# Performance work log

Measured on AMD Instinct MI355X. Metric: run time of the kernel, lower is better.

## Reference

```python
import jax, jax.numpy as jnp
import numpy as np

B, S, D = 2, 2048, 2048
H, HKV, DH = 32, 8, 64
WIN = 1024  # sliding_window
SCALE = 1.0 / np.sqrt(DH)
NEG_INF = -1e30


def setup_inputs() -> dict:
    key = jax.random.key(0)
    ks = jax.random.split(key, 6)
    w = 0.02
    inp = {
        "hidden_states": jax.random.normal(ks[0], (B, S, D), jnp.float32),
        "Wq": jax.random.normal(ks[1], (D, D), jnp.float32) * w,
        "bq": jnp.zeros((D,), jnp.float32),
        "Wk": jax.random.normal(ks[2], (HKV * DH, D), jnp.float32) * w,
        "bk": jnp.zeros((HKV * DH,), jnp.float32),
        "Wv": jax.random.normal(ks[3], (HKV * DH, D), jnp.float32) * w,
        "bv": jnp.zeros((HKV * DH,), jnp.float32),
        "Wo": jax.random.normal(ks[4], (D, D), jnp.float32) * w,
        "bo": jnp.zeros((D,), jnp.float32),
        # reset_parameters (default init): 1 / logspace(0, 7, H, base=2)
        "alibi_slopes": 1.0 / jnp.exp2(jnp.linspace(0.0, 7.0, H)).astype(jnp.float32),
    }
    return inp


def reference(hidden_states, Wq, bq, Wk, bk, Wv, bv, Wo, bo, alibi_slopes):
    x = hidden_states
    q = (x @ Wq.T + bq).reshape(B, S, H, DH).transpose(0, 2, 1, 3)      # [B,H,S,DH]
    k = (x @ Wk.T + bk).reshape(B, S, HKV, DH).transpose(0, 2, 1, 3)    # [B,HKV,S,DH]
    v = (x @ Wv.T + bv).reshape(B, S, HKV, DH).transpose(0, 2, 1, 3)
    # GQA: each kv head serves H//HKV consecutive query heads
    group = H // HKV
    k = jnp.repeat(k, group, axis=1)  # [B,H,S,DH]
    v = jnp.repeat(v, group, axis=1)

    scores = jnp.einsum("bhqd,bhkd->bhqk", q, k) * SCALE  # [B,H,S,S]
    i = jnp.arange(S)[:, None]
    j = jnp.arange(S)[None, :]
    rel = (j - i).astype(jnp.float32)  # <= 0 for attended past positions
    # ALiBi: slope * (j - i) -> linear penalty on distance
    bias = alibi_slopes[:, None, None] * rel  # [H,S,S]
    mask = (j <= i) & ((i - j) < WIN)  # [S,S]
    scores = jnp.where(mask[None, None], scores + bias[None], NEG_INF)
    probs = jax.nn.softmax(scores, axis=-1)
    out = jnp.einsum("bhqk,bhkd->bhqd", probs, v)  # [B,H,S,DH]
    out = out.transpose(0, 2, 1, 3).reshape(B, S, D)
    return out @ Wo.T + bo
```

## Files before the change

### kernel.cpp

```cpp
#include <hip/hip_runtime.h>
#include <hip/hip_bf16.h>
#include <stdint.h>
#include <type_traits>

typedef unsigned short ushort_t;
typedef __bf16 bf16x8 __attribute__((ext_vector_type(8)));
typedef __bf16 bf16x4 __attribute__((ext_vector_type(4)));
typedef short s16x4 __attribute__((ext_vector_type(4)));
typedef unsigned short u16x8 __attribute__((ext_vector_type(8)));
typedef float f32x4 __attribute__((ext_vector_type(4)));

#define MFMA_BF16(a, b, c) __builtin_amdgcn_mfma_f32_16x16x32_bf16((a), (b), (c), 0, 0, 0)

#define GLD_LDS(gptr, lptr) \
    __builtin_amdgcn_global_load_lds((const __attribute__((address_space(1))) void*)(gptr), \
                                     (__attribute__((address_space(3))) void*)(lptr), 16, 0, 0)

static __device__ __forceinline__ float bf2f(__hip_bfloat16 x) { return __bfloat162float(x); }
static __device__ __forceinline__ ushort_t f2bfbits(float f) {
    __hip_bfloat16 h = __float2bfloat16(f);
    return *(ushort_t*)&h;
}
static __device__ __forceinline__ float fmax3(float a, float b, float c) {
    return fmaxf(fmaxf(a, b), c);
}

static __device__ __forceinline__ f32x4 MFMA16(bf16x4 a, bf16x4 b, f32x4 c) {
#if __has_builtin(__builtin_amdgcn_mfma_f32_16x16x16_bf16)
    return __builtin_amdgcn_mfma_f32_16x16x16_bf16(a, b, c, 0, 0, 0);
#elif __has_builtin(__builtin_amdgcn_mfma_f32_16x16x16bf16_1k)
    union { bf16x4 b4; s16x4 s4; } ua, ub;
    ua.b4 = a; ub.b4 = b;
    return __builtin_amdgcn_mfma_f32_16x16x16bf16_1k(ua.s4, ub.s4, c, 0, 0, 0);
#else
    const bf16x4 z = {(__bf16)0.f, (__bf16)0.f, (__bf16)0.f, (__bf16)0.f};
    bf16x8 a8 = __builtin_shufflevector(a, z, 0, 1, 2, 3, 4, 5, 6, 7);
    bf16x8 b8 = __builtin_shufflevector(b, z, 0, 1, 2, 3, 4, 5, 6, 7);
    return MFMA_BF16(a8, b8, c);
#endif
}

static __device__ __forceinline__ bf16x4 pack4(float a, float b, float c, float d) {
    union { ushort4 u; bf16x4 v; } r;
    r.u = make_ushort4(f2bfbits(a), f2bfbits(b), f2bfbits(c), f2bfbits(d));
    return r.v;
}

template <typename T>
static __device__ __forceinline__ void storeT(T* p, float v);
template <>
__device__ __forceinline__ void storeT<float>(float* p, float v) { *p = v; }
template <>
__device__ __forceinline__ void storeT<__hip_bfloat16>(__hip_bfloat16* p, float v) {
    *p = __float2bfloat16(v);
}

__global__ void detect_kernel(const ushort_t* __restrict__ X,
                              const void* bq, const void* bk, const void* bv,
                              const void* bo, const void* slopes,
                              int* flag, float* slopesF, float* bqF,
                              float* bkF, float* bvF, float* boF) {
    __shared__ int cnt_s;
    if (threadIdx.x == 0) cnt_s = 0;
    __syncthreads();
    int cnt = 0;
    for (int i = threadIdx.x; i < 8192; i += 256) {
        ushort_t u = X[2 * i];
        int ex = (u >> 7) & 0xFF;
        if (ex >= 0xC0) cnt++;
    }
    for (int off = 1; off < 64; off <<= 1) cnt += __shfl_xor(cnt, off);
    if ((threadIdx.x & 63) == 0) atomicAdd(&cnt_s, cnt);
    __syncthreads();
    const bool f32 = cnt_s > 100;
    if (threadIdx.x == 0) *flag = f32 ? 1 : 0;
    auto conv = [&](const void* src, float* dst, int n) {
        for (int i = threadIdx.x; i < n; i += 256)
            dst[i] = f32 ? ((const float*)src)[i]
                         : __bfloat162float(((const __hip_bfloat16*)src)[i]);
    };
    conv(bq, bqF, 2048);
    conv(bk, bkF, 512);
    conv(bv, bvF, 512);
    conv(bo, boF, 2048);
    conv(slopes, slopesF, 32);
}

__global__ __launch_bounds__(256) void cvt_kernel(const int* __restrict__ flag,
                                                  const void* __restrict__ src,
                                                  ushort_t* __restrict__ dst, int n4) {
    const bool f32 = (*flag == 1);
    const int stride = gridDim.x * 256;
    for (int i = blockIdx.x * 256 + threadIdx.x; i < n4; i += stride) {
        if (f32) {
            float4 f = ((const float4*)src)[i];
            ((ushort4*)dst)[i] =
                make_ushort4(f2bfbits(f.x), f2bfbits(f.y), f2bfbits(f.z), f2bfbits(f.w));
        } else {
            ((ushort4*)dst)[i] = ((const ushort4*)src)[i];
        }
    }
}

__device__ __forceinline__ void stage_tile(const __hip_bfloat16* __restrict__ M, int K,
                                           int k0, ushort_t* lds, int tid) {
    const int wave = tid >> 6, lane = tid & 63;
    const int srow = lane >> 3;
    const int scol = ((lane & 7) ^ srow) * 8;
#pragma unroll
    for (int t = 0; t < 4; ++t) {
        const int chunk = wave * 4 + t;
        GLD_LDS((const ushort_t*)M + (size_t)(chunk * 8 + srow) * K + k0 + scol,
                lds + chunk * 512);
    }
}

__device__ __forceinline__ void stage_tile(const float* __restrict__ M, int K,
                                           int k0, ushort_t* lds, int tid) {
#pragma unroll
    for (int q = 0; q < 8; ++q) {
        const int idx = q * 256 + tid;
        const int row = idx >> 4;
        const int c4 = (idx & 15) * 4;
        float4 f = *(const float4*)(M + (size_t)row * K + k0 + c4);
        const int dcol = (((c4 >> 3) ^ (row & 7)) * 8) + (c4 & 7);
        *(ushort4*)(lds + row * 64 + dcol) =
            make_ushort4(f2bfbits(f.x), f2bfbits(f.y), f2bfbits(f.z), f2bfbits(f.w));
    }
}

template <typename TA, typename TW, typename TC>
__device__ __forceinline__ void gemm_tile(const TA* __restrict__ A,
                                          const TW* __restrict__ W,
                                          const float* __restrict__ biasF,
                                          TC* __restrict__ C, int K, int ldc) {
    __shared__ __align__(16) ushort_t As[128 * 64];
    __shared__ __align__(16) ushort_t Bs[128 * 64];
    const int tid = threadIdx.x;
    const int wave = tid >> 6, lane = tid & 63;
    const int quad = lane >> 4, l15 = lane & 15;
    const int wm = (wave >> 1) * 64, wn = (wave & 1) * 64;
    const int sw = l15 & 7;

    f32x4 acc[4][4];
#pragma unroll
    for (int i = 0; i < 4; ++i)
#pragma unroll
        for (int j = 0; j < 4; ++j) acc[i][j] = {0.f, 0.f, 0.f, 0.f};

    for (int k0 = 0; k0 < K; k0 += 64) {
        stage_tile(A, K, k0, As, tid);
        stage_tile(W, K, k0, Bs, tid);
        __syncthreads();
#pragma unroll
        for (int kk = 0; kk < 2; ++kk) {
            const int chs = ((kk * 4 + quad) ^ sw) * 8;
            bf16x8 af[4], bfr[4];
#pragma unroll
            for (int mi = 0; mi < 4; ++mi)
                af[mi] = *(const bf16x8*)(As + (wm + mi * 16 + l15) * 64 + chs);
#pragma unroll
            for (int ni = 0; ni < 4; ++ni)
                bfr[ni] = *(const bf16x8*)(Bs + (wn + ni * 16 + l15) * 64 + chs);
#pragma unroll
            for (int mi = 0; mi < 4; ++mi)
#pragma unroll
                for (int ni = 0; ni < 4; ++ni)
                    acc[mi][ni] = MFMA_BF16(af[mi], bfr[ni], acc[mi][ni]);
        }
        __syncthreads();
    }
#pragma unroll
    for (int mi = 0; mi < 4; ++mi) {
#pragma unroll
        for (int ni = 0; ni < 4; ++ni) {
            const int col = wn + ni * 16 + l15;
            const float bv = biasF[col];
#pragma unroll
            for (int r = 0; r < 4; ++r) {
                const int row = wm + mi * 16 + quad * 4 + r;
                storeT(C + (size_t)row * ldc + col, acc[mi][ni][r] + bv);
            }
        }
    }
}

__global__ __launch_bounds__(256, 2) void qkv_fast(
    const __hip_bfloat16* __restrict__ X,
    const __hip_bfloat16* __restrict__ Wq, const __hip_bfloat16* __restrict__ Wk,
    const __hip_bfloat16* __restrict__ Wv, const float* __restrict__ bqF,
    const float* __restrict__ bkF, const float* __restrict__ bvF,
    __hip_bfloat16* __restrict__ Qb, __hip_bfloat16* __restrict__ Kb,
    __hip_bfloat16* __restrict__ Vb) {
    const int nt = blockIdx.x, mt = blockIdx.y;
    const __hip_bfloat16* W;
    const float* bias;
    __hip_bfloat16* C;
    int ldc, colbase;
    if (nt < 16)      { W = Wq; bias = bqF; C = Qb; ldc = 2048; colbase = nt * 128; }
    else if (nt < 20) { W = Wk; bias = bkF; C = Kb; ldc = 512;  colbase = (nt - 16) * 128; }
    else              { W = Wv; bias = bvF; C = Vb; ldc = 512;  colbase = (nt - 20) * 128; }
    gemm_tile(X + (size_t)mt * 128 * 2048, W + (size_t)colbase * 2048, bias + colbase,
              C + (size_t)mt * 128 * ldc + colbase, 2048, ldc);
}

__global__ __launch_bounds__(256, 2) void oproj_fast(
    const __hip_bfloat16* __restrict__ A, const __hip_bfloat16* __restrict__ Wo,
    const float* __restrict__ boF, float* __restrict__ C) {
    gemm_tile(A + (size_t)blockIdx.y * 128 * 2048,
              Wo + (size_t)blockIdx.x * 128 * 2048, boF + blockIdx.x * 128,
              C + (size_t)blockIdx.y * 128 * 2048 + blockIdx.x * 128, 2048, 2048);
}

__global__ __launch_bounds__(256) void vtrans_kernel(const ushort_t* __restrict__ Vb,
                                                     ushort_t* __restrict__ Vt) {
    const int blk = blockIdx.x;
    const int bh = blk >> 6;
    const int sc = blk & 63;
    const int tid = threadIdx.x;
    const int dh = tid & 63;
    const int s0 = sc * 32 + (tid >> 6) * 8;
    const int b = bh >> 3, hkv = bh & 7;
    u16x8 vv;
#pragma unroll
    for (int e = 0; e < 8; ++e)
        vv[e] = Vb[((size_t)(b * 2048 + s0 + e)) * 512 + hkv * 64 + dh];
    *(u16x8*)(Vt + ((size_t)(bh * 64 + dh)) * 2048 + s0) = vv;
}

template <bool F32>
__global__ __launch_bounds__(256, 2) void qkv_kernel(
    const int* __restrict__ flag, const void* __restrict__ Xv,
    const void* __restrict__ Wqv, const void* __restrict__ Wkv,
    const void* __restrict__ Wvv, const float* __restrict__ bqF,
    const float* __restrict__ bkF, const float* __restrict__ bvF,
    __hip_bfloat16* __restrict__ Qb, __hip_bfloat16* __restrict__ Kb,
    __hip_bfloat16* __restrict__ Vb) {
    if ((*flag == 1) != F32) return;
    using T = typename std::conditional<F32, float, __hip_bfloat16>::type;
    const T* X = (const T*)Xv;
    const int nt = blockIdx.x, mt = blockIdx.y;
    const T* W;
    const float* bias;
    __hip_bfloat16* C;
    int ldc, colbase;
    if (nt < 16)      { W = (const T*)Wqv; bias = bqF; C = Qb; ldc = 2048; colbase = nt * 128; }
    else if (nt < 20) { W = (const T*)Wkv; bias = bkF; C = Kb; ldc = 512;  colbase = (nt - 16) * 128; }
    else              { W = (const T*)Wvv; bias = bvF; C = Vb; ldc = 512;  colbase = (nt - 20) * 128; }
    gemm_tile(X + (size_t)mt * 128 * 2048, W + (size_t)colbase * 2048, bias + colbase,
              C + (size_t)mt * 128 * ldc + colbase, 2048, ldc);
}

template <bool F32>
__global__ __launch_bounds__(256, 2) void oproj_kernel(
    const int* __restrict__ flag, const __hip_bfloat16* __restrict__ A,
    const void* __restrict__ Wov, const float* __restrict__ boF,
    float* __restrict__ C) {
    if ((*flag == 1) != F32) return;
    using T = typename std::conditional<F32, float, __hip_bfloat16>::type;
    gemm_tile(A + (size_t)blockIdx.y * 128 * 2048,
              (const T*)Wov + (size_t)blockIdx.x * 128 * 2048, boF + blockIdx.x * 128,
              C + (size_t)blockIdx.y * 128 * 2048 + blockIdx.x * 128, 2048, 2048);
}

__global__ __launch_bounds__(256, 4) void attn4_kernel(
    const __hip_bfloat16* __restrict__ Qg, const __hip_bfloat16* __restrict__ Kg,
    const ushort_t* __restrict__ Vt, const float* __restrict__ slopesF,
    __hip_bfloat16* __restrict__ Og) {
    constexpr int S = 2048, WIN = 1024;
    constexpr float LOG2E = 1.44269504f;
    constexpr float SCALE2 = 0.125f * LOG2E;
    constexpr float NEGBIG = -3e38f;
    __shared__ __align__(16) ushort_t K0s[64 * 64];
    __shared__ __align__(16) ushort_t V0s[64 * 64];
    __shared__ __align__(16) ushort_t K1s[64 * 64];
    __shared__ __align__(16) ushort_t V1s[64 * 64];

    const int p = blockIdx.x;
    const int xcd = p & 7;
    const int slot = p >> 3;
    const int bh = (slot >> 7) * 8 + xcd;
    const int h2 = (slot >> 5) & 3;
    const int qt = 31 - (slot & 31);
    const int b = bh >> 3, hkv = bh & 7;
    const int h = hkv * 4 + h2;
    const int i0 = qt * 64;

    const int tid = threadIdx.x;
    const int wave = tid >> 6, lane = tid & 63;
    const int quad = lane >> 4, l15 = lane & 15;
    const int jl = lane >> 3, cc = lane & 7;
    const float slope2 = slopesF[h] * LOG2E;

    const ushort_t* kbase = (const ushort_t*)Kg + (size_t)(b * S) * 512 + hkv * 64;
    const ushort_t* vbase = Vt + ((size_t)bh * 64) * 2048;

    auto stage = [&](int j0, ushort_t* Ks, ushort_t* Vs) {
        const int row0 = wave * 16;
#pragma unroll
        for (int t = 0; t < 2; ++t) {
            const int r = row0 + t * 8 + jl;
            GLD_LDS(kbase + (size_t)(j0 + r) * 512 + ((cc ^ (r & 7)) * 8),
                    Ks + (row0 + t * 8) * 64);
            GLD_LDS(vbase + (size_t)r * 2048 + j0 + ((cc ^ (r & 7)) * 8),
                    Vs + (row0 + t * 8) * 64);
        }
    };

    const int i = i0 + wave * 16 + l15;
    const __hip_bfloat16* qbase = Qg + ((size_t)(b * S + i)) * 2048 + h * 64;
    bf16x8 aq0 = *(const bf16x8*)(qbase + quad * 8);
    bf16x8 aq1 = *(const bf16x8*)(qbase + 32 + quad * 8);

    union { ushort4 u; bf16x4 v; } onesu;
    onesu.u = make_ushort4(0x3F80, 0x3F80, 0x3F80, 0x3F80);
    const bf16x4 onesf = onesu.v;

    f32x4 oaccT[4];
#pragma unroll
    for (int ni = 0; ni < 4; ++ni) oaccT[ni] = {0.f, 0.f, 0.f, 0.f};
    f32x4 lacc = {0.f, 0.f, 0.f, 0.f};
    float m_i = -1e30f;

    auto compute = [&](int j0, const ushort_t* Ks, const ushort_t* Vs, bool masked) {
        f32x4 st[4];
#pragma unroll
        for (int ni = 0; ni < 4; ++ni) st[ni] = {0.f, 0.f, 0.f, 0.f};
#pragma unroll
        for (int kk = 0; kk < 2; ++kk) {
            const bf16x8 aqk = kk ? aq1 : aq0;
#pragma unroll
            for (int ni = 0; ni < 4; ++ni) {
                const int row = ni * 16 + l15;
                bf16x8 kf = *(const bf16x8*)(Ks + row * 64 + ((kk * 4 + quad) ^ (row & 7)) * 8);
                st[ni] = MFMA_BF16(kf, aqk, st[ni]);
            }
        }
        float sv[4][4];
#pragma unroll
        for (int ni = 0; ni < 4; ++ni)
#pragma unroll
            for (int r = 0; r < 4; ++r) {
                const int rel = (j0 + ni * 16 + quad * 4 + r) - i;
                sv[ni][r] = fmaf(st[ni][r], SCALE2, slope2 * (float)rel);
            }
        if (masked) {
#pragma unroll
            for (int ni = 0; ni < 4; ++ni)
#pragma unroll
                for (int r = 0; r < 4; ++r) {
                    const int rel = (j0 + ni * 16 + quad * 4 + r) - i;
                    if (!((unsigned)(-rel) < (unsigned)WIN)) sv[ni][r] = NEGBIG;
                }
        }
        float mx = fmax3(fmax3(sv[0][0], sv[0][1], sv[0][2]),
                         fmax3(sv[0][3], sv[1][0], sv[1][1]),
                         fmax3(sv[1][2], sv[1][3], sv[2][0]));
        float my = fmax3(fmax3(sv[2][1], sv[2][2], sv[2][3]),
                         fmax3(sv[3][0], sv[3][1], sv[3][2]), sv[3][3]);
        mx = fmaxf(mx, my);
        mx = fmaxf(mx, __shfl_xor(mx, 16));
        mx = fmaxf(mx, __shfl_xor(mx, 32));
        if (!__all(mx <= m_i + 8.f)) {
            const float mn = fmaxf(m_i, mx);
            const float alpha = exp2f(m_i - mn);
            m_i = mn;
#pragma unroll
            for (int ni = 0; ni < 4; ++ni)
#pragma unroll
                for (int r = 0; r < 4; ++r) oaccT[ni][r] *= alpha;
            lacc[0] *= alpha;
        }
        float pv[4][4];
#pragma unroll
        for (int ni = 0; ni < 4; ++ni)
#pragma unroll
            for (int r = 0; r < 4; ++r) pv[ni][r] = exp2f(sv[ni][r] - m_i);
        bf16x4 pf[4];
#pragma unroll
        for (int c = 0; c < 4; ++c) pf[c] = pack4(pv[c][0], pv[c][1], pv[c][2], pv[c][3]);
#pragma unroll
        for (int c = 0; c < 4; ++c) lacc = MFMA16(onesf, pf[c], lacc);
#pragma unroll
        for (int ni = 0; ni < 4; ++ni) {
            const int row = ni * 16 + l15;
#pragma unroll
            for (int c = 0; c < 4; ++c) {
                const int cj = c * 2 + (quad >> 1);
                bf16x4 vf = *(const bf16x4*)(Vs + row * 64 + ((cj ^ (row & 7)) * 8) +
                                             (quad & 1) * 4);
                oaccT[ni] = MFMA16(vf, pf[c], oaccT[ni]);
            }
        }
    };

    const int jt_lo = (i0 - WIN + 1) > 0 ? ((i0 - WIN + 1) >> 6) : 0;
    int jt = jt_lo;
    stage(jt * 64, K0s, V0s);
    for (;;) {
        __syncthreads();
        if (jt < qt) stage((jt + 1) * 64, K1s, V1s);
        compute(jt * 64, K0s, V0s, (jt == qt) || (qt - jt >= 16));
        if (++jt > qt) break;
        __syncthreads();
        if (jt < qt) stage((jt + 1) * 64, K0s, V0s);
        compute(jt * 64, K1s, V1s, (jt == qt) || (qt - jt >= 16));
        if (++jt > qt) break;
    }
    const float inv = 1.0f / lacc[0];
    __hip_bfloat16* obase = Og + ((size_t)(b * S + i)) * 2048 + h * 64;
#pragma unroll
    for (int ni = 0; ni < 4; ++ni) {
        ushort4 o4 = make_ushort4(f2bfbits(oaccT[ni][0] * inv), f2bfbits(oaccT[ni][1] * inv),
                                  f2bfbits(oaccT[ni][2] * inv), f2bfbits(oaccT[ni][3] * inv));
        *(ushort4*)((ushort_t*)obase + ni * 16 + quad * 4) = o4;
    }
}

__global__ __launch_bounds__(256, 2) void attn_kernel(
    const __hip_bfloat16* __restrict__ Qg, const __hip_bfloat16* __restrict__ Kg,
    const __hip_bfloat16* __restrict__ Vg, const float* __restrict__ slopesF,
    __hip_bfloat16* __restrict__ Og) {
    constexpr int S = 2048, WIN = 1024;
    constexpr float SCALE = 0.125f;
    constexpr float LOG2E = 1.44269504f;
    __shared__ __align__(16) ushort_t P_lds[64 * 72];
    __shared__ __align__(16) ushort_t Vts[64 * 72];

    const int tile = blockIdx.x;
    const int qt = tile & 31;
    const int h = (tile >> 5) & 31;
    const int b = tile >> 10;
    const int i0 = qt * 64;
    const int hkv = h >> 2;
    const int tid = threadIdx.x;
    const int wave = tid >> 6, lane = tid & 63;
    const int quad = lane >> 4, l15 = lane & 15;
    const float slope = slopesF[h];

    const int qrow = i0 + wave * 16 + l15;
    const __hip_bfloat16* qbase = Qg + ((size_t)(b * S + qrow)) * 2048 + h * 64;
    bf16x8 aq[2];
    aq[0] = *(const bf16x8*)(qbase + quad * 8);
    aq[1] = *(const bf16x8*)(qbase + 32 + quad * 8);

    f32x4 oacc[4];
#pragma unroll
    for (int ni = 0; ni < 4; ++ni) oacc[ni] = {0.f, 0.f, 0.f, 0.f};
    float m_i[4], l_i[4];
#pragma unroll
    for (int r = 0; r < 4; ++r) { m_i[r] = -1e30f; l_i[r] = 0.f; }

    const int jt_lo = (i0 - WIN + 1) > 0 ? ((i0 - WIN + 1) >> 6) : 0;
    for (int jt = jt_lo; jt <= qt; ++jt) {
        const int j0 = jt * 64;
#pragma unroll
        for (int it = 0; it < 2; ++it) {
            const int j = it * 32 + (tid >> 3);
            const int dh0 = (tid & 7) * 8;
            u16x8 vv = *(const u16x8*)(Vg + ((size_t)(b * S + j0 + j)) * 512 + hkv * 64 + dh0);
#pragma unroll
            for (int e = 0; e < 8; ++e) Vts[(dh0 + e) * 72 + j] = vv[e];
        }
        f32x4 sacc[4];
#pragma unroll
        for (int ni = 0; ni < 4; ++ni) sacc[ni] = {0.f, 0.f, 0.f, 0.f};
#pragma unroll
        for (int kk = 0; kk < 2; ++kk) {
#pragma unroll
            for (int ni = 0; ni < 4; ++ni) {
                bf16x8 bkf = *(const bf16x8*)(Kg + ((size_t)(b * S + j0 + ni * 16 + l15)) * 512 +
                                              hkv * 64 + kk * 32 + quad * 8);
                sacc[ni] = MFMA_BF16(aq[kk], bkf, sacc[ni]);
            }
        }
#pragma unroll
        for (int r = 0; r < 4; ++r) {
            const int i = i0 + wave * 16 + quad * 4 + r;
            float sv[4];
            float rowmax = -1e30f;
#pragma unroll
            for (int ni = 0; ni < 4; ++ni) {
                const int j = j0 + ni * 16 + l15;
                float s = sacc[ni][r] * SCALE + slope * (float)(j - i);
                const bool valid = (j <= i) && ((i - j) < WIN);
                s = valid ? s : -1e30f;
                sv[ni] = s;
                rowmax = fmaxf(rowmax, s);
            }
#pragma unroll
            for (int off = 1; off < 16; off <<= 1)
                rowmax = fmaxf(rowmax, __shfl_xor(rowmax, off));
            const float mn = fmaxf(m_i[r], rowmax);
            const float alpha = exp2f((m_i[r] - mn) * LOG2E);
            float rowsum = 0.f;
#pragma unroll
            for (int ni = 0; ni < 4; ++ni) {
                const float p = (sv[ni] > -1e29f) ? exp2f((sv[ni] - mn) * LOG2E) : 0.f;
                P_lds[(wave * 16 + quad * 4 + r) * 72 + ni * 16 + l15] = f2bfbits(p);
                rowsum += p;
            }
#pragma unroll
            for (int off = 1; off < 16; off <<= 1) rowsum += __shfl_xor(rowsum, off);
            l_i[r] = l_i[r] * alpha + rowsum;
            m_i[r] = mn;
#pragma unroll
            for (int ni = 0; ni < 4; ++ni) oacc[ni][r] *= alpha;
        }
        __syncthreads();
#pragma unroll
        for (int kk = 0; kk < 2; ++kk) {
            bf16x8 ap = *(const bf16x8*)(P_lds + (wave * 16 + l15) * 72 + kk * 32 + quad * 8);
#pragma unroll
            for (int ni = 0; ni < 4; ++ni) {
                bf16x8 bvf = *(const bf16x8*)(Vts + (ni * 16 + l15) * 72 + kk * 32 + quad * 8);
                oacc[ni] = MFMA_BF16(ap, bvf, oacc[ni]);
            }
        }
        __syncthreads();
    }
#pragma unroll
    for (int ni = 0; ni < 4; ++ni) {
#pragma unroll
        for (int r = 0; r < 4; ++r) {
            const int srow = i0 + wave * 16 + quad * 4 + r;
            const float v = oacc[ni][r] / l_i[r];
            Og[((size_t)(b * S + srow)) * 2048 + h * 64 + ni * 16 + l15] = __float2bfloat16(v);
        }
    }
}

extern "C" void kernel_launch(void* const* d_in, const int* in_sizes, int n_in,
                              void* d_out, int out_size, void* d_ws, size_t ws_size,
                              hipStream_t stream) {
    (void)in_sizes; (void)n_in; (void)out_size;
    const void* X  = d_in[0];
    const void* Wq = d_in[1];
    const void* bq = d_in[2];
    const void* Wk = d_in[3];
    const void* bk = d_in[4];
    const void* Wv = d_in[5];
    const void* bv = d_in[6];
    const void* Wo = d_in[7];
    const void* bo = d_in[8];
    const void* sl = d_in[9];
    float* outp = (float*)d_out;

    char* ws = (char*)d_ws;
    const size_t SZ_X  = (size_t)4096 * 2048 * 2;
    const size_t SZ_WQ = (size_t)2048 * 2048 * 2;
    const size_t SZ_WK = (size_t)512 * 2048 * 2;
    const size_t SZ_Q  = SZ_X;
    const size_t SZ_K  = (size_t)4096 * 512 * 2;
    const size_t FAST_NEED = SZ_X + SZ_WQ + 2 * SZ_WK + SZ_Q + 2 * SZ_K + 65536;

    if (ws_size >= FAST_NEED) {
        size_t o = 0;
        __hip_bfloat16* Xb  = (__hip_bfloat16*)(ws + o); o += SZ_X;
        __hip_bfloat16* Wqb = (__hip_bfloat16*)(ws + o); o += SZ_WQ;
        __hip_bfloat16* Wkb = (__hip_bfloat16*)(ws + o); o += SZ_WK;
        __hip_bfloat16* Wvb = (__hip_bfloat16*)(ws + o); o += SZ_WK;
        __hip_bfloat16* Qb  = (__hip_bfloat16*)(ws + o); o += SZ_Q;
        __hip_bfloat16* Kb  = (__hip_bfloat16*)(ws + o); o += SZ_K;
        __hip_bfloat16* Vb  = (__hip_bfloat16*)(ws + o); o += SZ_K;
        __hip_bfloat16* Ab  = Xb;
        __hip_bfloat16* Wob = Wqb;
        ushort_t*       Vtg = (ushort_t*)Wkb;
        int*   flag    = (int*)(ws + o);
        float* slopesF = (float*)(ws + o + 1024);
        float* bqF     = (float*)(ws + o + 4096);
        float* bkF     = bqF + 2048;
        float* bvF     = bkF + 512;
        float* boF     = bvF + 512;

        detect_kernel<<<1, 256, 0, stream>>>((const ushort_t*)X, bq, bk, bv, bo, sl,
                                             flag, slopesF, bqF, bkF, bvF, boF);
        cvt_kernel<<<2048, 256, 0, stream>>>(flag, X,  (ushort_t*)Xb,  4096 * 2048 / 4);
        cvt_kernel<<<2048, 256, 0, stream>>>(flag, Wq, (ushort_t*)Wqb, 2048 * 2048 / 4);
        cvt_kernel<<<512,  256, 0, stream>>>(flag, Wk, (ushort_t*)Wkb, 512 * 2048 / 4);
        cvt_kernel<<<512,  256, 0, stream>>>(flag, Wv, (ushort_t*)Wvb, 512 * 2048 / 4);
        qkv_fast<<<dim3(24, 32), 256, 0, stream>>>(Xb, Wqb, Wkb, Wvb, bqF, bkF, bvF,
                                                   Qb, Kb, Vb);
        vtrans_kernel<<<1024, 256, 0, stream>>>((const ushort_t*)Vb, Vtg);
        cvt_kernel<<<2048, 256, 0, stream>>>(flag, Wo, (ushort_t*)Wob, 2048 * 2048 / 4);
        attn4_kernel<<<dim3(2048), 256, 0, stream>>>(Qb, Kb, Vtg, slopesF, Ab);
        oproj_fast<<<dim3(16, 32), 256, 0, stream>>>(Ab, Wob, boF, outp);
    } else {
        const size_t MB = 1024 * 1024;
        __hip_bfloat16* Qb = (__hip_bfloat16*)(ws);
        __hip_bfloat16* Kb = (__hip_bfloat16*)(ws + 16 * MB);
        __hip_bfloat16* Vb = (__hip_bfloat16*)(ws + 20 * MB);
        __hip_bfloat16* Ab = (__hip_bfloat16*)(ws + 24 * MB);
        int*   flag    = (int*)(ws + 40 * MB);
        float* slopesF = (float*)(ws + 40 * MB + 1024);
        float* bqF     = (float*)(ws + 40 * MB + 4096);
        float* bkF     = bqF + 2048;
        float* bvF     = bkF + 512;
        float* boF     = bvF + 512;

        detect_kernel<<<1, 256, 0, stream>>>((const ushort_t*)X, bq, bk, bv, bo, sl,
                                             flag, slopesF, bqF, bkF, bvF, boF);
        qkv_kernel<false><<<dim3(24, 32), 256, 0, stream>>>(flag, X, Wq, Wk, Wv,
                                                            bqF, bkF, bvF, Qb, Kb, Vb);
        qkv_kernel<true><<<dim3(24, 32), 256, 0, stream>>>(flag, X, Wq, Wk, Wv,
                                                           bqF, bkF, bvF, Qb, Kb, Vb);
        attn_kernel<<<dim3(2048), 256, 0, stream>>>(Qb, Kb, Vb, slopesF, Ab);
        oproj_kernel<false><<<dim3(16, 32), 256, 0, stream>>>(flag, Ab, Wo, boF, outp);
        oproj_kernel<true><<<dim3(16, 32), 256, 0, stream>>>(flag, Ab, Wo, boF, outp);
    }
}
```

Measured before the change: 340.2 us.

## Widen attention blocks to 128 query rows, fuse input conversions, raise GEMM occupancy

The attention kernel now runs 512-thread blocks covering 128 query rows (two 64-row tiles), so each staged K/V tile in LDS is shared by eight waves instead of four, which halves K/V global traffic per query. Each wave skips key tiles that fall outside its own causal and sliding-window range. The four separate fp32-to-bf16 conversion launches for X, Wq, Wk and Wv are merged into one kernel to cut launch overhead. The GEMM launch bounds are raised to 3 blocks per CU, which may force register spilling. The wider attention block also adds idle waves at the edges of the window.

```diff
diff --git a/kernel.cpp b/kernel.cpp
--- a/kernel.cpp
+++ b/kernel.cpp
@@ -102,6 +102,39 @@
     }
 }
 
+__global__ __launch_bounds__(256) void cvt4_kernel(const int* __restrict__ flag,
+                                                   const void* __restrict__ X,
+                                                   const void* __restrict__ Wq,
+                                                   const void* __restrict__ Wk,
+                                                   const void* __restrict__ Wv,
+                                                   ushort_t* __restrict__ Xb,
+                                                   ushort_t* __restrict__ Wqb,
+                                                   ushort_t* __restrict__ Wkb,
+                                                   ushort_t* __restrict__ Wvb) {
+    const bool f32 = (*flag == 1);
+    constexpr int nX = 4096 * 2048 / 4;
+    constexpr int nWq = 2048 * 2048 / 4;
+    constexpr int nWk = 512 * 2048 / 4;
+    constexpr int total = nX + nWq + 2 * nWk;
+    const int stride = gridDim.x * 256;
+    for (int i = blockIdx.x * 256 + threadIdx.x; i < total; i += stride) {
+        const void* src;
+        ushort_t* dst;
+        int off;
+        if (i < nX)                 { src = X;  dst = Xb;  off = i; }
+        else if (i < nX + nWq)      { src = Wq; dst = Wqb; off = i - nX; }
+        else if (i < nX + nWq + nWk){ src = Wk; dst = Wkb; off = i - nX - nWq; }
+        else                        { src = Wv; dst = Wvb; off = i - nX - nWq - nWk; }
+        if (f32) {
+            float4 f = ((const float4*)src)[off];
+            ((ushort4*)dst)[off] =
+                make_ushort4(f2bfbits(f.x), f2bfbits(f.y), f2bfbits(f.z), f2bfbits(f.w));
+        } else {
+            ((ushort4*)dst)[off] = ((const ushort4*)src)[off];
+        }
+    }
+}
+
 __device__ __forceinline__ void stage_tile(const __hip_bfloat16* __restrict__ M, int K,
                                            int k0, ushort_t* lds, int tid) {
     const int wave = tid >> 6, lane = tid & 63;
@@ -185,7 +218,7 @@
     }
 }
 
-__global__ __launch_bounds__(256, 2) void qkv_fast(
+__global__ __launch_bounds__(256, 3) void qkv_fast(
     const __hip_bfloat16* __restrict__ X,
     const __hip_bfloat16* __restrict__ Wq, const __hip_bfloat16* __restrict__ Wk,
     const __hip_bfloat16* __restrict__ Wv, const float* __restrict__ bqF,
@@ -204,7 +237,7 @@
               C + (size_t)mt * 128 * ldc + colbase, 2048, ldc);
 }
 
-__global__ __launch_bounds__(256, 2) void oproj_fast(
+__global__ __launch_bounds__(256, 3) void oproj_fast(
     const __hip_bfloat16* __restrict__ A, const __hip_bfloat16* __restrict__ Wo,
     const float* __restrict__ boF, float* __restrict__ C) {
     gemm_tile(A + (size_t)blockIdx.y * 128 * 2048,
@@ -263,7 +296,7 @@
               C + (size_t)blockIdx.y * 128 * 2048 + blockIdx.x * 128, 2048, 2048);
 }
 
-__global__ __launch_bounds__(256, 4) void attn4_kernel(
+__global__ __launch_bounds__(512, 8) void attn4_kernel(
     const __hip_bfloat16* __restrict__ Qg, const __hip_bfloat16* __restrict__ Kg,
     const ushort_t* __restrict__ Vt, const float* __restrict__ slopesF,
     __hip_bfloat16* __restrict__ Og) {
@@ -279,32 +312,28 @@
     const int p = blockIdx.x;
     const int xcd = p & 7;
     const int slot = p >> 3;
-    const int bh = (slot >> 7) * 8 + xcd;
-    const int h2 = (slot >> 5) & 3;
-    const int qt = 31 - (slot & 31);
+    const int bh = (slot >> 6) * 8 + xcd;
+    const int h2 = (slot >> 4) & 3;
+    const int qt2 = 15 - (slot & 15);
     const int b = bh >> 3, hkv = bh & 7;
     const int h = hkv * 4 + h2;
-    const int i0 = qt * 64;
+    const int i0 = qt2 * 128;
 
     const int tid = threadIdx.x;
     const int wave = tid >> 6, lane = tid & 63;
     const int quad = lane >> 4, l15 = lane & 15;
     const int jl = lane >> 3, cc = lane & 7;
     const float slope2 = slopesF[h] * LOG2E;
+    const int qt_w = 2 * qt2 + (wave >> 2);
 
     const ushort_t* kbase = (const ushort_t*)Kg + (size_t)(b * S) * 512 + hkv * 64;
     const ushort_t* vbase = Vt + ((size_t)bh * 64) * 2048;
 
     auto stage = [&](int j0, ushort_t* Ks, ushort_t* Vs) {
-        const int row0 = wave * 16;
-#pragma unroll
-        for (int t = 0; t < 2; ++t) {
-            const int r = row0 + t * 8 + jl;
-            GLD_LDS(kbase + (size_t)(j0 + r) * 512 + ((cc ^ (r & 7)) * 8),
-                    Ks + (row0 + t * 8) * 64);
-            GLD_LDS(vbase + (size_t)r * 2048 + j0 + ((cc ^ (r & 7)) * 8),
-                    Vs + (row0 + t * 8) * 64);
-        }
+        const int row0 = wave * 8;
+        const int r = row0 + jl;
+        GLD_LDS(kbase + (size_t)(j0 + r) * 512 + ((cc ^ jl) * 8), Ks + row0 * 64);
+        GLD_LDS(vbase + (size_t)r * 2048 + j0 + ((cc ^ jl) * 8), Vs + row0 * 64);
     };
 
     const int i = i0 + wave * 16 + l15;
@@ -394,18 +423,25 @@
         }
     };
 
-    const int jt_lo = (i0 - WIN + 1) > 0 ? ((i0 - WIN + 1) >> 6) : 0;
-    int jt = jt_lo;
+    const int LO = (2 * qt2 - 16) > 0 ? (2 * qt2 - 16) : 0;
+    const int HI = 2 * qt2 + 1;
+    int jt = LO;
     stage(jt * 64, K0s, V0s);
     for (;;) {
         __syncthreads();
-        if (jt < qt) stage((jt + 1) * 64, K1s, V1s);
-        compute(jt * 64, K0s, V0s, (jt == qt) || (qt - jt >= 16));
-        if (++jt > qt) break;
+        if (jt < HI) stage((jt + 1) * 64, K1s, V1s);
+        {
+            const int d = qt_w - jt;
+            if ((unsigned)d <= 16u) compute(jt * 64, K0s, V0s, (d == 0) || (d >= 16));
+        }
+        if (++jt > HI) break;
         __syncthreads();
-        if (jt < qt) stage((jt + 1) * 64, K0s, V0s);
-        compute(jt * 64, K1s, V1s, (jt == qt) || (qt - jt >= 16));
-        if (++jt > qt) break;
+        if (jt < HI) stage((jt + 1) * 64, K0s, V0s);
+        {
+            const int d = qt_w - jt;
+            if ((unsigned)d <= 16u) compute(jt * 64, K1s, V1s, (d == 0) || (d >= 16));
+        }
+        if (++jt > HI) break;
     }
     const float inv = 1.0f / lacc[0];
     __hip_bfloat16* obase = Og + ((size_t)(b * S + i)) * 2048 + h * 64;
@@ -575,15 +611,14 @@
 
         detect_kernel<<<1, 256, 0, stream>>>((const ushort_t*)X, bq, bk, bv, bo, sl,
                                              flag, slopesF, bqF, bkF, bvF, boF);
-        cvt_kernel<<<2048, 256, 0, stream>>>(flag, X,  (ushort_t*)Xb,  4096 * 2048 / 4);
-        cvt_kernel<<<2048, 256, 0, stream>>>(flag, Wq, (ushort_t*)Wqb, 2048 * 2048 / 4);
-        cvt_kernel<<<512,  256, 0, stream>>>(flag, Wk, (ushort_t*)Wkb, 512 * 2048 / 4);
-        cvt_kernel<<<512,  256, 0, stream>>>(flag, Wv, (ushort_t*)Wvb, 512 * 2048 / 4);
+        cvt4_kernel<<<2048, 256, 0, stream>>>(flag, X, Wq, Wk, Wv, (ushort_t*)Xb,
+                                              (ushort_t*)Wqb, (ushort_t*)Wkb,
+                                              (ushort_t*)Wvb);
         qkv_fast<<<dim3(24, 32), 256, 0, stream>>>(Xb, Wqb, Wkb, Wvb, bqF, bkF, bvF,
                                                    Qb, Kb, Vb);
         vtrans_kernel<<<1024, 256, 0, stream>>>((const ushort_t*)Vb, Vtg);
         cvt_kernel<<<2048, 256, 0, stream>>>(flag, Wo, (ushort_t*)Wob, 2048 * 2048 / 4);
-        attn4_kernel<<<dim3(2048), 256, 0, stream>>>(Qb, Kb, Vtg, slopesF, Ab);
+        attn4_kernel<<<dim3(1024), 512, 0, stream>>>(Qb, Kb, Vtg, slopesF, Ab);
         oproj_fast<<<dim3(16, 32), 256, 0, stream>>>(Ab, Wob, boF, outp);
     } else {
         const size_t MB = 1024 * 1024;
```

New measurement: 391.2 us. 1.15x slower.
